# Kernel tuning notes

Hardware: AMD Instinct MI355X
Metric: run time of the kernel (lower is better)

The kernel has to match this reference:

```python
import jax, jax.numpy as jnp
import numpy as np

N_ATOMS, N_EDGES, N_TRIP, N_GRAPHS = 8000, 100000, 500000, 64
H, NR, NS, NB = 128, 6, 7, 8
NBLK, OUT, NBEF, NAFT, NOL = 6, 1, 1, 2, 3


def setup_inputs() -> dict:
    key = jax.random.key(0)
    ks = iter(jax.random.split(key, 64))

    def nrm(shape, s=0.1):
        return jax.random.normal(next(ks), shape, jnp.float32) * s

    def rint(shape, hi):
        return jax.random.randint(next(ks), shape, 0, hi)

    return dict(
        z=rint((N_ATOMS,), 95),
        rbf=nrm((N_EDGES, NR), 1.0),
        sbf=nrm((N_TRIP, NS * NR), 1.0),
        i=rint((N_EDGES,), N_ATOMS),
        j=rint((N_EDGES,), N_ATOMS),
        idx_kj=rint((N_TRIP,), N_EDGES),
        idx_ji=rint((N_TRIP,), N_EDGES),
        batch=jnp.sort(rint((N_ATOMS,), N_GRAPHS)),
        emb_table=nrm((95, H), 1.0),
        emb_rbf_w=nrm((NR, H)), emb_rbf_b=nrm((H,), 0.01),
        emb_w=nrm((3 * H, H)), emb_b=nrm((H,), 0.01),
        int_rbf_w=nrm((NBLK, NR, H)),
        int_sbf_w=nrm((NBLK, NS * NR, NB)),
        int_kj_w=nrm((NBLK, H, H)), int_kj_b=nrm((NBLK, H), 0.01),
        int_ji_w=nrm((NBLK, H, H)), int_ji_b=nrm((NBLK, H), 0.01),
        int_W=nrm((NBLK, H, NB, H), 2.0 / H),
        int_bef_w=nrm((NBLK, 2 * NBEF, H, H)), int_bef_b=nrm((NBLK, 2 * NBEF, H), 0.01),
        int_lin_w=nrm((NBLK, H, H)), int_lin_b=nrm((NBLK, H), 0.01),
        int_aft_w=nrm((NBLK, 2 * NAFT, H, H)), int_aft_b=nrm((NBLK, 2 * NAFT, H), 0.01),
        out_rbf_w=nrm((NBLK + 1, NR, H)),
        out_lins_w=nrm((NBLK + 1, NOL, H, H)), out_lins_b=nrm((NBLK + 1, NOL, H), 0.01),
        out_w=nrm((NBLK + 1, H, OUT)),
    )


def _forward(z, i, j, idx_kj, idx_ji, batch,
             rbf, sbf, emb_table, emb_rbf_w, emb_rbf_b, emb_w, emb_b,
             int_rbf_w, int_sbf_w, int_kj_w, int_kj_b, int_ji_w, int_ji_b,
             int_W, int_bef_w, int_bef_b, int_lin_w, int_lin_b,
             int_aft_w, int_aft_b, out_rbf_w, out_lins_w, out_lins_b, out_w):
    act = jax.nn.silu  # swish

    def residual(h, ws, bs):
        # ws: [2*n_layers, H, H] -> x + act(lin2(act(lin1(x)))) per layer
        for r in range(ws.shape[0] // 2):
            h = h + act(act(h @ ws[2 * r] + bs[2 * r]) @ ws[2 * r + 1] + bs[2 * r + 1])
        return h

    def out_block(xe, k):
        t = (rbf @ out_rbf_w[k]) * xe                      # [E,H]
        t = jax.ops.segment_sum(t, i, num_segments=N_ATOMS)  # edge->node scatter
        for l in range(NOL):
            t = act(t @ out_lins_w[k, l] + out_lins_b[k, l])
        return t @ out_w[k]                                # [N,OUT]

    # EmbeddingBlock
    h_atom = emb_table[z]                                  # [N,H]
    rbf_h = act(rbf @ emb_rbf_w + emb_rbf_b)               # [E,H]
    x = act(jnp.concatenate([h_atom[i], h_atom[j], rbf_h], axis=-1) @ emb_w + emb_b)  # [E,H]

    P = out_block(x, 0)
    for b in range(NBLK):
        rbf_p = rbf @ int_rbf_w[b]                         # [E,H]
        sbf_p = sbf @ int_sbf_w[b]                         # [T,NB]
        x_ji = act(x @ int_ji_w[b] + int_ji_b[b])
        x_kj = act(x @ int_kj_w[b] + int_kj_b[b]) * rbf_p
        xg = x_kj[idx_kj]                                  # triplet gather [T,H]
        # einsum('wj,wl,ijl->wi', sbf_p, xg, W): loop over small NB to avoid [T,NB,H] temp
        Wb = int_W[b]                                      # [H,NB,H]
        m = sbf_p[:, 0:1] * (xg @ Wb[:, 0, :].T)
        for jj in range(1, NB):
            m = m + sbf_p[:, jj:jj + 1] * (xg @ Wb[:, jj, :].T)
        m = jax.ops.segment_sum(m, idx_ji, num_segments=N_EDGES)  # triplet->edge scatter
        h = x_ji + m
        h = residual(h, int_bef_w[b], int_bef_b[b])
        h = act(h @ int_lin_w[b] + int_lin_b[b]) + x       # skip connection
        x = residual(h, int_aft_w[b], int_aft_b[b])
        P = P + out_block(x, b + 1)

    return jax.ops.segment_sum(P, batch, num_segments=N_GRAPHS)  # [B,OUT]


def reference(z, rbf, sbf, i, j, idx_kj, idx_ji, batch,
              emb_table, emb_rbf_w, emb_rbf_b, emb_w, emb_b,
              int_rbf_w, int_sbf_w, int_kj_w, int_kj_b, int_ji_w, int_ji_b,
              int_W, int_bef_w, int_bef_b, int_lin_w, int_lin_b,
              int_aft_w, int_aft_b, out_rbf_w, out_lins_w, out_lins_b, out_w):
    return _forward(z, i, j, idx_kj, idx_ji, batch,
                    rbf, sbf, emb_table, emb_rbf_w, emb_rbf_b, emb_w, emb_b,
                    int_rbf_w, int_sbf_w, int_kj_w, int_kj_b, int_ji_w, int_ji_b,
                    int_W, int_bef_w, int_bef_b, int_lin_w, int_lin_b,
                    int_aft_w, int_aft_b, out_rbf_w, out_lins_w, out_lins_b, out_w)
```

## Files before the change

kernel.cpp:

```cpp
#include <hip/hip_runtime.h>
#include <cstdint>
#include <cstddef>

typedef unsigned short ushort_t;
typedef unsigned int uint_t;

#define NATOMS 8000
#define NEDGES 100000
#define NTRIP  500000
#define NGRAPH 64
#define HD     128
#define NRR    6
#define NSNR   42
#define NBB    8
#define NBLKS  6
#define MSZ    16384

using short8   = __attribute__((ext_vector_type(8))) short;
using ushort8v = __attribute__((ext_vector_type(8))) unsigned short;
using floatx4  = __attribute__((ext_vector_type(4))) float;
using float2v  = __attribute__((ext_vector_type(2))) float;

__device__ __forceinline__ float siluf(float x){ return x / (1.f + __expf(-x)); }
__device__ __forceinline__ ushort_t f2us(float f){
    uint_t u = __builtin_bit_cast(uint_t, f);
    u = (u + 0x7FFFu + ((u >> 16) & 1u)) >> 16;
    return (ushort_t)u;
}
__device__ __forceinline__ float us2f(ushort_t s){
    uint_t u = ((uint_t)s) << 16;
    return __builtin_bit_cast(float, u);
}
__device__ __forceinline__ void wave_lds_fence(){
    asm volatile("s_waitcnt lgkmcnt(0)" ::: "memory");
}
__device__ __forceinline__ short8 ldfrag(const ushort_t* W, int frag, int lane){
    return *(const short8*)(W + ((size_t)(frag * 64 + lane) << 3));
}

__global__ void zerof_k(float* __restrict__ p, int n){ int i=blockIdx.x*256+threadIdx.x; if(i<n) p[i]=0.f; }
__global__ void zeroi_k(int* __restrict__ p, int n){ int i=blockIdx.x*256+threadIdx.x; if(i<n) p[i]=0; }

__global__ __launch_bounds__(256)
void transp128_k(const float* __restrict__ src, ushort_t* __restrict__ dst)
{
    __shared__ ushort_t L[128][130];
    int m = blockIdx.x;
    const float* S = src + (size_t)m * MSZ;
    ushort_t* D = dst + (size_t)m * MSZ;
    int tid = threadIdx.x;
    #pragma unroll
    for (int p = 0; p < 64; ++p) {
        int idx = p * 256 + tid;
        int k = idx >> 7, n = idx & 127;
        L[k][n] = f2us(S[idx]);
    }
    __syncthreads();
    #pragma unroll
    for (int p = 0; p < 64; ++p) {
        int idx = p * 256 + tid;
        int n = idx >> 7, k = idx & 127;
        D[idx] = L[k][n];
    }
}

__global__ __launch_bounds__(256)
void transp128s_k(const float* __restrict__ src, ushort_t* __restrict__ dst)
{
    int m = blockIdx.x;
    const float* S = src + (size_t)m * MSZ;
    ushort_t* D = dst + (size_t)m * MSZ;
    int tid = threadIdx.x;
    #pragma unroll
    for (int p = 0; p < 64; ++p) {
        int idx = p * 256 + tid;
        int k = idx >> 7, n = idx & 127;
        size_t d = ((size_t)(((k >> 5) * 8 + (n >> 4)) * 64 + ((k >> 3) & 3) * 16 + (n & 15)) << 3)
                   + (k & 7);
        D[d] = f2us(S[idx]);
    }
}

__global__ void castWMs_k(const float* __restrict__ src, ushort_t* __restrict__ dst, int n)
{
    int i = blockIdx.x * 256 + threadIdx.x;
    if (i >= n) return;
    int b = i >> 17;
    int r = i & 131071;
    int nn = r >> 10, k = r & 1023;
    size_t d = (size_t)b * 131072
             + ((size_t)(((k >> 5) * 8 + (nn >> 4)) * 64 + ((k >> 3) & 3) * 16 + (nn & 15)) << 3)
             + (k & 7);
    dst[d] = f2us(src[i]);
}

__global__ void pack_bc_k(const float* __restrict__ bef, const float* __restrict__ lin,
                          const float* __restrict__ aft, float* __restrict__ bc)
{
    int b = blockIdx.x;
    for (int i = threadIdx.x; i < 7 * HD; i += 256) {
        int s = i >> 7, h = i & 127;
        float v;
        if (s < 2)      v = bef[(size_t)(b * 2 + s) * HD + h];
        else if (s == 2) v = lin[(size_t)b * HD + h];
        else             v = aft[(size_t)(b * 4 + (s - 3)) * HD + h];
        bc[(size_t)b * 7 * HD + i] = v;
    }
}

__global__ void hist_k(const int* __restrict__ idx, int n, int* __restrict__ cnt)
{
    int i = blockIdx.x * 256 + threadIdx.x;
    if (i < n) atomicAdd(&cnt[idx[i]], 1);
}
__global__ void blksum_k(const int* __restrict__ c, int n, int* __restrict__ bs)
{
    int i = blockIdx.x * 256 + threadIdx.x;
    int v = (i < n) ? c[i] : 0;
    #pragma unroll
    for (int off = 32; off; off >>= 1) v += __shfl_down(v, off);
    __shared__ int sh[4];
    if ((threadIdx.x & 63) == 0) sh[threadIdx.x >> 6] = v;
    __syncthreads();
    if (threadIdx.x == 0) bs[blockIdx.x] = sh[0] + sh[1] + sh[2] + sh[3];
}
__global__ void scanb_k(int* __restrict__ bs, int nb)
{
    __shared__ int sh[1024];
    int t = threadIdx.x;
    int v = (t < nb) ? bs[t] : 0;
    sh[t] = v; __syncthreads();
    for (int off = 1; off < 1024; off <<= 1) {
        int u = (t >= off) ? sh[t - off] : 0;
        __syncthreads();
        sh[t] += u;
        __syncthreads();
    }
    if (t < nb) bs[t] = sh[t] - v;
}
__global__ void scanfin_k(const int* __restrict__ c, int n, const int* __restrict__ bs,
                          int* __restrict__ offs)
{
    __shared__ int sh[256];
    int t = threadIdx.x;
    int i = blockIdx.x * 256 + t;
    int v = (i < n) ? c[i] : 0;
    sh[t] = v; __syncthreads();
    for (int off = 1; off < 256; off <<= 1) {
        int u = (t >= off) ? sh[t - off] : 0;
        __syncthreads();
        sh[t] += u;
        __syncthreads();
    }
    if (i < n)  offs[i] = bs[blockIdx.x] + sh[t] - v;
    if (i == n - 1) offs[n] = bs[blockIdx.x] + sh[t];
}
__global__ void fill_k(const int* __restrict__ idx, int n, const int* __restrict__ offs,
                       int* __restrict__ cur, int* __restrict__ sorted)
{
    int i = blockIdx.x * 256 + threadIdx.x;
    if (i >= n) return;
    int e = idx[i];
    int p = offs[e] + atomicAdd(&cur[e], 1);
    sorted[p] = i;
}
__global__ void invperm_k(const int* __restrict__ tsorted, const int* __restrict__ idx_kj,
                          int* __restrict__ tpos, int* __restrict__ ekjs, int n)
{
    int k = blockIdx.x * 256 + threadIdx.x;
    if (k >= n) return;
    int t = tsorted[k];
    tpos[t] = k;
    ekjs[k] = idx_kj[t];
}

__device__ __forceinline__ void load_bh(const ushort_t* Bt, int kh, int tid, ushort8v r[4])
{
    #pragma unroll
    for (int p = 0; p < 4; ++p) {
        int c = p * 256 + tid;
        int n = c >> 3, c8 = c & 7;
        r[p] = *(const ushort8v*)(Bt + (size_t)n * 128 + kh * 64 + c8 * 8);
    }
}
__device__ __forceinline__ void store_bh(ushort8v r[4], ushort_t (*Bl)[72], int tid)
{
    #pragma unroll
    for (int p = 0; p < 4; ++p) {
        int c = p * 256 + tid;
        *(ushort8v*)&Bl[c >> 3][(c & 7) * 8] = r[p];
    }
}
__device__ __forceinline__ void mfma_kh(ushort_t (*Al)[136], ushort_t (*Bl)[72],
                                        floatx4 acc[4][4], int kh,
                                        int wr, int wc, int lhi, int llo)
{
    #pragma unroll
    for (int ks = 0; ks < 2; ++ks) {
        int kk = ks * 32 + lhi * 8;
        short8 af[4], bf[4];
        #pragma unroll
        for (int tm = 0; tm < 4; ++tm)
            af[tm] = *(const short8*)&Al[wr * 64 + tm * 16 + llo][kh * 64 + kk];
        #pragma unroll
        for (int tn = 0; tn < 4; ++tn)
            bf[tn] = *(const short8*)&Bl[wc * 64 + tn * 16 + llo][kk];
        #pragma unroll
        for (int tm = 0; tm < 4; ++tm)
            #pragma unroll
            for (int tn = 0; tn < 4; ++tn)
                acc[tm][tn] = __builtin_amdgcn_mfma_f32_16x16x32_bf16(
                    af[tm], bf[tn], acc[tm][tn], 0, 0, 0);
    }
}
#define ZERO_ACC4(acc) { _Pragma("unroll") for (int a_=0;a_<4;++a_) _Pragma("unroll") \
    for (int b_=0;b_<4;++b_) _Pragma("unroll") for (int q_=0;q_<4;++q_) acc[a_][b_][q_]=0.f; }
#define ZERO_ACC8(acc) { _Pragma("unroll") for (int t_=0;t_<8;++t_) { acc[t_][0]=0.f; acc[t_][1]=0.f; acc[t_][2]=0.f; acc[t_][3]=0.f; } }

__global__ __launch_bounds__(256)
void emb_chain_k(const float* __restrict__ rbf, const float* __restrict__ W6g,
                 const float* __restrict__ b6g, const ushort_t* __restrict__ Wemb3,
                 const float* __restrict__ A0, const float* __restrict__ A1,
                 const float* __restrict__ emb_b, const int* __restrict__ z,
                 const int* __restrict__ ii, const int* __restrict__ jj,
                 float* __restrict__ X, ushort_t* __restrict__ Xb, int M)
{
    __shared__ ushort_t Al[128][136];
    __shared__ ushort_t Bl[128][72];
    __shared__ float W6[NRR * HD];
    __shared__ float b6s[HD];
    const int tid = threadIdx.x, row0 = blockIdx.x * 128;
    const int wave = tid >> 6, lane = tid & 63;
    const int wr = wave >> 1, wc_ = wave & 1, lhi = lane >> 4, llo = lane & 15;

    for (int i = tid; i < NRR * HD; i += 256) W6[i] = W6g[i];
    if (tid < HD) b6s[tid] = b6g[tid];
    ushort8v r0[4], r1[4];
    load_bh(Wemb3, 0, tid, r0); load_bh(Wemb3, 1, tid, r1);
    __syncthreads();

    {
        int e_l = tid >> 1, half = tid & 1;
        int grow = row0 + e_l; if (grow >= M) grow = M - 1;
        float r6[NRR];
        #pragma unroll
        for (int r = 0; r < NRR; ++r) r6[r] = rbf[(size_t)grow * NRR + r];
        #pragma unroll 8
        for (int hh = 0; hh < 64; ++hh) {
            int h = half * 64 + hh;
            float a = b6s[h];
            #pragma unroll
            for (int r = 0; r < NRR; ++r) a += r6[r] * W6[r * HD + h];
            Al[e_l][h] = f2us(siluf(a));
        }
    }
    __syncthreads();

    floatx4 acc[4][4]; ZERO_ACC4(acc);
    store_bh(r0, Bl, tid); __syncthreads();
    mfma_kh(Al, Bl, acc, 0, wr, wc_, lhi, llo);
    __syncthreads();
    store_bh(r1, Bl, tid); __syncthreads();
    mfma_kh(Al, Bl, acc, 1, wr, wc_, lhi, llo);

    #pragma unroll
    for (int tm = 0; tm < 4; ++tm)
        #pragma unroll
        for (int q = 0; q < 4; ++q) {
            int grow = row0 + wr * 64 + tm * 16 + lhi * 4 + q;
            if (grow >= M) continue;
            int zi = z[ii[grow]], zj = z[jj[grow]];
            #pragma unroll
            for (int tn = 0; tn < 4; ++tn) {
                int coll = wc_ * 64 + tn * 16 + llo;
                float t = acc[tm][tn][q] + A0[zi * HD + coll] + A1[zj * HD + coll] + emb_b[coll];
                float v = siluf(t);
                size_t o = (size_t)grow * HD + coll;
                X[o] = v; Xb[o] = f2us(v);
            }
        }
}

__global__ __launch_bounds__(256, 3)
void kjcb_w(const ushort_t* __restrict__ Xb, const ushort_t* __restrict__ Wkj,
            const float* __restrict__ bkj, const float* __restrict__ rbf,
            const float* __restrict__ Wr6, ushort_t* __restrict__ Cb, int M)
{
    __shared__ float W6s[NRR * HD];
    __shared__ float bkjS[HD];
    const int tid = threadIdx.x, wave = tid >> 6, lane = tid & 63;
    const int llo = lane & 15, lhi = lane >> 4;
    for (int i = tid; i < NRR * HD; i += 256) W6s[i] = Wr6[i];
    if (tid < HD) bkjS[tid] = bkj[tid];
    __syncthreads();
    const int row0 = (blockIdx.x * 4 + wave) * 16;
    if (row0 >= M) return;

    short8 af[4];
    #pragma unroll
    for (int kc = 0; kc < 4; ++kc)
        af[kc] = *(const short8*)(Xb + (size_t)(row0 + llo) * HD + kc * 32 + lhi * 8);

    short8 nb[2][8];
    #pragma unroll
    for (int d = 0; d < 2; ++d)
        #pragma unroll
        for (int tn = 0; tn < 8; ++tn) nb[d][tn] = ldfrag(Wkj, d * 8 + tn, lane);

    float rb[4][NRR];
    {
        const float* rp = rbf + (size_t)(row0 + lhi * 4) * NRR;
        #pragma unroll
        for (int q = 0; q < 4; ++q)
            #pragma unroll
            for (int r = 0; r < NRR; ++r) rb[q][r] = rp[q * NRR + r];
    }

    floatx4 acc[8]; ZERO_ACC8(acc);
    #pragma unroll
    for (int kc = 0; kc < 4; ++kc) {
        short8 bq[8];
        #pragma unroll
        for (int tn = 0; tn < 8; ++tn) bq[tn] = nb[kc & 1][tn];
        if (kc + 2 < 4) {
            #pragma unroll
            for (int tn = 0; tn < 8; ++tn) nb[kc & 1][tn] = ldfrag(Wkj, (kc + 2) * 8 + tn, lane);
        }
        #pragma unroll
        for (int tn = 0; tn < 8; ++tn)
            acc[tn] = __builtin_amdgcn_mfma_f32_16x16x32_bf16(af[kc], bq[tn], acc[tn], 0, 0, 0);
    }
    #pragma unroll
    for (int tn = 0; tn < 8; ++tn) {
        int col = tn * 16 + llo;
        #pragma unroll
        for (int q = 0; q < 4; ++q) {
            int grow = row0 + lhi * 4 + q;
            if (grow >= M) continue;
            float rpv = 0.f;
            #pragma unroll
            for (int r = 0; r < NRR; ++r) rpv += rb[q][r] * W6s[r * HD + col];
            Cb[(size_t)grow * HD + col] = f2us(siluf(acc[tn][q] + bkjS[col]) * rpv);
        }
    }
}

__global__ __launch_bounds__(256, 4)
void megaK_w(const ushort_t* __restrict__ sps, const ushort_t* __restrict__ Cb,
             const int* __restrict__ toffs, const int* __restrict__ ekjs,
             const ushort_t* __restrict__ Xb,
             const ushort_t* __restrict__ Wm,
             const ushort_t* __restrict__ Wji, const float* __restrict__ bjig,
             const ushort_t* __restrict__ Wc, const float* __restrict__ Bc,
             float* __restrict__ X, ushort_t* __restrict__ Xbo)
{
    __shared__ ushort_t Ga[16384];
    const int tid = threadIdx.x, wave = tid >> 6, lane = tid & 63;
    const int llo = lane & 15, lhi = lane >> 4;
    const int tn0 = wave * 2, tn1 = tn0 + 1;
    const int col0 = tn0 * 16 + llo, col1 = tn1 * 16 + llo;

    const float bj0 = bjig[col0], bj1 = bjig[col1];
    float bsc0[7], bsc1[7];
    #pragma unroll
    for (int s = 0; s < 7; ++s) {
        bsc0[s] = Bc[s * HD + col0];
        bsc1[s] = Bc[s * HD + col1];
    }

    const int row0 = blockIdx.x * 16;

    {
        const int we0 = row0 + wave * 4;
        const int tf0 = __builtin_amdgcn_readfirstlane(toffs[we0]);
        const int tf1 = __builtin_amdgcn_readfirstlane(toffs[we0 + 1]);
        const int tf2 = __builtin_amdgcn_readfirstlane(toffs[we0 + 2]);
        const int tf3 = __builtin_amdgcn_readfirstlane(toffs[we0 + 3]);
        const int tf4 = __builtin_amdgcn_readfirstlane(toffs[we0 + 4]);
        const int wk0 = tf0, wk1 = tf4;
        const uint_t* __restrict__ Cb32 = (const uint_t*)Cb;

        float2v accp[8];
        #pragma unroll
        for (int j = 0; j < 8; ++j) accp[j] = (float2v){0.f, 0.f};

        int ekA[8]; uint_t cbuf[8]; ushort8v sbuf[8];
        #pragma unroll
        for (int p = 0; p < 8; ++p)
            ekA[p] = (wk0 + p < wk1) ? __builtin_amdgcn_readfirstlane(ekjs[wk0 + p]) : 0;
        #pragma unroll
        for (int p = 0; p < 8; ++p)
            if (wk0 + p < wk1) {
                cbuf[p] = Cb32[(size_t)ekA[p] * 64 + lane];
                sbuf[p] = *(const ushort8v*)(sps + (size_t)(wk0 + p) * NBB);
            }
        #pragma unroll
        for (int p = 0; p < 8; ++p)
            ekA[p] = (wk0 + 8 + p < wk1) ? __builtin_amdgcn_readfirstlane(ekjs[wk0 + 8 + p]) : 0;

        int e = 0;
        auto kendof = [&](int ee) {
            return ee == 0 ? tf1 : ee == 1 ? tf2 : ee == 2 ? tf3 : tf4;
        };
        auto flush = [&](int ee) {
            const int el_ = wave * 4 + ee;
            const int sw_ = (el_ & 7) << 3;
            const int gb_ = el_ << 10;
            const int cix = (2 * lane) ^ sw_;
            #pragma unroll
            for (int j = 0; j < 8; ++j) {
                uint_t pk = (uint_t)f2us(accp[j][0]) | ((uint_t)f2us(accp[j][1]) << 16);
                *(uint_t*)&Ga[gb_ + (j << 7) + cix] = pk;
                accp[j] = (float2v){0.f, 0.f};
            }
        };

        for (int base = wk0; base < wk1; base += 8) {
            #pragma unroll
            for (int p = 0; p < 8; ++p) {
                const int kk = base + p;
                if (kk < wk1) {
                    while (e < 4 && kk >= kendof(e)) { flush(e); ++e; }
                    const uint_t  cu = cbuf[p];
                    const ushort8v sv = sbuf[p];
                    if (kk + 8 < wk1) {
                        cbuf[p] = Cb32[(size_t)ekA[p] * 64 + lane];
                        sbuf[p] = *(const ushort8v*)(sps + (size_t)(kk + 8) * NBB);
                    }
                    if (kk + 16 < wk1)
                        ekA[p] = __builtin_amdgcn_readfirstlane(ekjs[kk + 16]);
                    const float2v c2 = { us2f((ushort_t)(cu & 0xffffu)),
                                         __builtin_bit_cast(float, cu & 0xffff0000u) };
                    #pragma unroll
                    for (int j = 0; j < 8; ++j) {
                        const float s = us2f(sv[j]);
                        accp[j] += (float2v){s, s} * c2;
                    }
                }
            }
        }
        while (e < 4) { flush(e); ++e; }
    }
    __syncthreads();

    floatx4 m0 = {0.f,0.f,0.f,0.f}, m1 = {0.f,0.f,0.f,0.f};
    {
        const int abase = llo << 10;
        const int aswz  = llo & 7;
        short8 ap[2]; short8 bp[4][2];
        #pragma unroll
        for (int d = 0; d < 2; ++d)
            ap[d] = *(const short8*)&Ga[abase + ((((d << 2) + lhi) ^ aswz) << 3)];
        #pragma unroll
        for (int d = 0; d < 4; ++d) {
            bp[d][0] = ldfrag(Wm, d * 8 + tn0, lane);
            bp[d][1] = ldfrag(Wm, d * 8 + tn1, lane);
        }
        __builtin_amdgcn_s_setprio(1);
        #pragma unroll
        for (int kc = 0; kc < 32; ++kc) {
            short8 a  = ap[kc & 1];
            short8 b0 = bp[kc & 3][0], b1 = bp[kc & 3][1];
            if (kc + 2 < 32)
                ap[kc & 1] = *(const short8*)&Ga[abase + (((((kc + 2) << 2) + lhi) ^ aswz) << 3)];
            if (kc + 4 < 32) {
                bp[kc & 3][0] = ldfrag(Wm, (kc + 4) * 8 + tn0, lane);
                bp[kc & 3][1] = ldfrag(Wm, (kc + 4) * 8 + tn1, lane);
            }
            m0 = __builtin_amdgcn_mfma_f32_16x16x32_bf16(a, b0, m0, 0, 0, 0);
            m1 = __builtin_amdgcn_mfma_f32_16x16x32_bf16(a, b1, m1, 0, 0, 0);
        }
        __builtin_amdgcn_s_setprio(0);
    }
    __syncthreads();

    ushort_t (*Tw)[136] = (ushort_t (*)[136])&Ga[0];

    float cur0[4], cur1[4], res0[4], res1[4], trk0[4], trk1[4];
    short8 nb[2][2];
    #pragma unroll
    for (int d = 0; d < 2; ++d) {
        nb[d][0] = ldfrag(Wji, d * 8 + tn0, lane);
        nb[d][1] = ldfrag(Wji, d * 8 + tn1, lane);
    }
    {
        short8 af[4];
        #pragma unroll
        for (int kc = 0; kc < 4; ++kc)
            af[kc] = *(const short8*)(Xb + (size_t)(row0 + llo) * HD + kc * 32 + lhi * 8);
        floatx4 a0 = {0.f,0.f,0.f,0.f}, a1 = {0.f,0.f,0.f,0.f};
        #pragma unroll
        for (int kc = 0; kc < 4; ++kc) {
            short8 b0 = nb[kc & 1][0], b1 = nb[kc & 1][1];
            {
                const int ps = kc + 2;
                const ushort_t* W = (ps < 4) ? Wji : Wc;
                nb[kc & 1][0] = ldfrag(W, (ps & 3) * 8 + tn0, lane);
                nb[kc & 1][1] = ldfrag(W, (ps & 3) * 8 + tn1, lane);
            }
            a0 = __builtin_amdgcn_mfma_f32_16x16x32_bf16(af[kc], b0, a0, 0, 0, 0);
            a1 = __builtin_amdgcn_mfma_f32_16x16x32_bf16(af[kc], b1, a1, 0, 0, 0);
        }
        #pragma unroll
        for (int q = 0; q < 4; ++q) {
            res0[q] = siluf(a0[q] + bj0) + m0[q];
            res1[q] = siluf(a1[q] + bj1) + m1[q];
            cur0[q] = res0[q]; cur1[q] = res1[q];
        }
    }

    float xr0[4], xr1[4];
    #pragma unroll
    for (int q = 0; q < 4; ++q) {
        int grow = row0 + lhi * 4 + q;
        xr0[q] = X[(size_t)grow * HD + col0];
        xr1[q] = X[(size_t)grow * HD + col1];
    }

    #pragma unroll
    for (int s = 0; s < 7; ++s) {
        #pragma unroll
        for (int q = 0; q < 4; ++q) {
            Tw[lhi * 4 + q][col0] = f2us(cur0[q]);
            Tw[lhi * 4 + q][col1] = f2us(cur1[q]);
        }
        __syncthreads();

        floatx4 a0 = {0.f,0.f,0.f,0.f}, a1 = {0.f,0.f,0.f,0.f};
        const int sg0 = 4 + s * 4;
        #pragma unroll
        for (int kc = 0; kc < 4; ++kc) {
            const int seg = sg0 + kc;
            short8 a8 = *(const short8*)&Tw[llo][kc * 32 + lhi * 8];
            short8 b0 = nb[seg & 1][0], b1 = nb[seg & 1][1];
            if (seg + 2 < 32) {
                const int ps = seg + 2;
                const ushort_t* W = Wc + (size_t)((ps - 4) >> 2) * MSZ;
                nb[seg & 1][0] = ldfrag(W, (ps & 3) * 8 + tn0, lane);
                nb[seg & 1][1] = ldfrag(W, (ps & 3) * 8 + tn1, lane);
            }
            a0 = __builtin_amdgcn_mfma_f32_16x16x32_bf16(a8, b0, a0, 0, 0, 0);
            a1 = __builtin_amdgcn_mfma_f32_16x16x32_bf16(a8, b1, a1, 0, 0, 0);
        }
        __syncthreads();

        #pragma unroll
        for (int q = 0; q < 4; ++q) {
            float t0v = siluf(a0[q] + bsc0[s]);
            float t1v = siluf(a1[q] + bsc1[s]);
            if (s == 0)      { cur0[q] = t0v; cur1[q] = t1v; }
            else if (s == 1) { cur0[q] = t0v + res0[q]; cur1[q] = t1v + res1[q]; }
            else if (s == 2) {
                cur0[q] = t0v + xr0[q];
                cur1[q] = t1v + xr1[q];
                trk0[q] = cur0[q]; trk1[q] = cur1[q];
            }
            else if (s == 3 || s == 5) { cur0[q] = t0v; cur1[q] = t1v; }
            else {
                cur0[q] = t0v + trk0[q]; cur1[q] = t1v + trk1[q];
                trk0[q] = cur0[q]; trk1[q] = cur1[q];
            }
        }
    }

    #pragma unroll
    for (int q = 0; q < 4; ++q) {
        int grow = row0 + lhi * 4 + q;
        size_t o = (size_t)grow * HD;
        X[o + col0] = cur0[q];        X[o + col1] = cur1[q];
        Xbo[o + col0] = f2us(cur0[q]); Xbo[o + col1] = f2us(cur1[q]);
    }
}

__global__ __launch_bounds__(256)
void gatherT_k(const ushort_t* __restrict__ Xb, const float* __restrict__ rbf,
               const float* __restrict__ Wr6, const int* __restrict__ eoffs,
               const int* __restrict__ esorted, ushort_t* __restrict__ TA, int M)
{
    __shared__ float W6s[NRR * HD];
    const int tid = threadIdx.x, wave = tid >> 6, lane = tid & 63;
    for (int i = tid; i < NRR * HD; i += 256) W6s[i] = Wr6[i];
    __syncthreads();
    int a0 = (blockIdx.x * 4 + wave) * 2;
    #pragma unroll
    for (int s = 0; s < 2; ++s) {
        int a = a0 + s;
        if (a >= M) return;
        float acc0 = 0.f, acc1 = 0.f;
        int k1 = eoffs[a + 1];
        for (int k = eoffs[a]; k < k1; ++k) {
            int e = esorted[k];
            float r6[NRR];
            #pragma unroll
            for (int r = 0; r < NRR; ++r) r6[r] = rbf[(size_t)e * NRR + r];
            float rp0 = 0.f, rp1 = 0.f;
            #pragma unroll
            for (int r = 0; r < NRR; ++r) {
                rp0 += r6[r] * W6s[r * HD + lane];
                rp1 += r6[r] * W6s[r * HD + 64 + lane];
            }
            acc0 += rp0 * us2f(Xb[(size_t)e * HD + lane]);
            acc1 += rp1 * us2f(Xb[(size_t)e * HD + 64 + lane]);
        }
        TA[(size_t)a * HD + lane] = f2us(acc0);
        TA[(size_t)a * HD + 64 + lane] = f2us(acc1);
    }
}

__global__ __launch_bounds__(256, 3)
void atomchain_w(const ushort_t* __restrict__ TA, const ushort_t* __restrict__ Wl,
                 const float* __restrict__ bl, const float* __restrict__ wout,
                 float* __restrict__ P, int M)
{
    __shared__ float blS[3 * HD];
    __shared__ float woS[HD];
    __shared__ ushort_t T[4][16][136];
    const int tid = threadIdx.x, wave = tid >> 6, lane = tid & 63;
    const int llo = lane & 15, lhi = lane >> 4;
    for (int i = tid; i < 3 * HD; i += 256) blS[i] = bl[i];
    if (tid < HD) woS[tid] = wout[tid];
    __syncthreads();
    const int row0 = (blockIdx.x * 4 + wave) * 16;
    if (row0 >= M) return;
    ushort_t (*Tw)[136] = T[wave];

    short8 nb[2][8];
    #pragma unroll
    for (int d = 0; d < 2; ++d)
        #pragma unroll
        for (int tn = 0; tn < 8; ++tn) nb[d][tn] = ldfrag(Wl, d * 8 + tn, lane);

    #pragma unroll
    for (int s = 0; s < 3; ++s) {
        short8 af[4];
        if (s == 0) {
            #pragma unroll
            for (int kc = 0; kc < 4; ++kc)
                af[kc] = *(const short8*)(TA + (size_t)(row0 + llo) * HD + kc * 32 + lhi * 8);
        } else {
            #pragma unroll
            for (int kc = 0; kc < 4; ++kc)
                af[kc] = *(const short8*)&Tw[llo][kc * 32 + lhi * 8];
        }
        floatx4 acc[8]; ZERO_ACC8(acc);
        #pragma unroll
        for (int kc = 0; kc < 4; ++kc) {
            const int seg = s * 4 + kc;
            short8 bq[8];
            #pragma unroll
            for (int tn = 0; tn < 8; ++tn) bq[tn] = nb[seg & 1][tn];
            if (seg + 2 < 12) {
                const int ps = seg + 2;
                const ushort_t* W = Wl + (size_t)(ps >> 2) * MSZ;
                #pragma unroll
                for (int tn = 0; tn < 8; ++tn)
                    nb[seg & 1][tn] = ldfrag(W, (ps & 3) * 8 + tn, lane);
            }
            #pragma unroll
            for (int tn = 0; tn < 8; ++tn)
                acc[tn] = __builtin_amdgcn_mfma_f32_16x16x32_bf16(af[kc], bq[tn], acc[tn], 0, 0, 0);
        }
        if (s < 2) {
            wave_lds_fence();
            #pragma unroll
            for (int tn = 0; tn < 8; ++tn) {
                int col = tn * 16 + llo;
                #pragma unroll
                for (int q = 0; q < 4; ++q)
                    Tw[lhi * 4 + q][col] = f2us(siluf(acc[tn][q] + blS[s * HD + col]));
            }
            wave_lds_fence();
        } else {
            #pragma unroll
            for (int q = 0; q < 4; ++q) {
                float v = 0.f;
                #pragma unroll
                for (int tn = 0; tn < 8; ++tn) {
                    int col = tn * 16 + llo;
                    v += siluf(acc[tn][q] + blS[2 * HD + col]) * woS[col];
                }
                v += __shfl_xor(v, 1); v += __shfl_xor(v, 2);
                v += __shfl_xor(v, 4); v += __shfl_xor(v, 8);
                int a = row0 + lhi * 4 + q;
                if (llo == 0 && a < M) P[a] += v;
            }
        }
    }
}

__global__ void emb_lin_k(const float* __restrict__ emb_table, const float* __restrict__ emb_w,
                          float* __restrict__ A0, float* __restrict__ A1)
{
    __shared__ float er[HD];
    int a = blockIdx.x, h = threadIdx.x;
    er[h] = emb_table[a * HD + h];
    __syncthreads();
    float acc0 = 0.f, acc1 = 0.f;
    #pragma unroll 8
    for (int l = 0; l < HD; ++l) {
        float e = er[l];
        acc0 += e * emb_w[l * HD + h];
        acc1 += e * emb_w[(HD + l) * HD + h];
    }
    A0[a * HD + h] = acc0;
    A1[a * HD + h] = acc1;
}

__global__ void sbf_proj_s(const float* __restrict__ sbf, const float* __restrict__ W,
                           const int* __restrict__ tpos, ushort_t* __restrict__ sps)
{
    __shared__ float Ws[NSNR * NBB];
    for (int s = threadIdx.x; s < NSNR * NBB; s += 256) Ws[s] = W[s];
    __syncthreads();
    int t = blockIdx.x * 256 + threadIdx.x;
    if (t >= NTRIP) return;
    float acc[NBB];
    #pragma unroll
    for (int n = 0; n < NBB; ++n) acc[n] = 0.f;
    #pragma unroll
    for (int r = 0; r < NSNR; ++r) {
        float v = sbf[(size_t)t * NSNR + r];
        #pragma unroll
        for (int n = 0; n < NBB; ++n) acc[n] += v * Ws[r * NBB + n];
    }
    int p = tpos[t];
    ushort_t* o = sps + (size_t)p * NBB;
    #pragma unroll
    for (int n = 0; n < NBB; ++n) o[n] = f2us(acc[n]);
}

__global__ void graph_sum_k(const float* __restrict__ P, const int* __restrict__ batch,
                            float* __restrict__ outg)
{
    int a = blockIdx.x * 256 + threadIdx.x;
    if (a >= NATOMS) return;
    atomicAdd(&outg[batch[a]], P[a]);
}

extern "C" void kernel_launch(void* const* d_in, const int* in_sizes, int n_in,
                              void* d_out, int out_size, void* d_ws, size_t ws_size,
                              hipStream_t stream)
{
    const int*   z         = (const int*)  d_in[0];
    const float* rbf       = (const float*)d_in[1];
    const float* sbf       = (const float*)d_in[2];
    const int*   ii        = (const int*)  d_in[3];
    const int*   jj        = (const int*)  d_in[4];
    const int*   idx_kj    = (const int*)  d_in[5];
    const int*   idx_ji    = (const int*)  d_in[6];
    const int*   batch     = (const int*)  d_in[7];
    const float* emb_table = (const float*)d_in[8];
    const float* emb_rbf_w = (const float*)d_in[9];
    const float* emb_rbf_b = (const float*)d_in[10];
    const float* emb_w     = (const float*)d_in[11];
    const float* emb_b     = (const float*)d_in[12];
    const float* int_rbf_w = (const float*)d_in[13];
    const float* int_sbf_w = (const float*)d_in[14];
    const float* int_kj_w  = (const float*)d_in[15];
    const float* int_kj_b  = (const float*)d_in[16];
    const float* int_ji_w  = (const float*)d_in[17];
    const float* int_ji_b  = (const float*)d_in[18];
    const float* int_W     = (const float*)d_in[19];
    const float* int_bef_w = (const float*)d_in[20];
    const float* int_bef_b = (const float*)d_in[21];
    const float* int_lin_w = (const float*)d_in[22];
    const float* int_lin_b = (const float*)d_in[23];
    const float* int_aft_w = (const float*)d_in[24];
    const float* int_aft_b = (const float*)d_in[25];
    const float* out_rbf_w = (const float*)d_in[26];
    const float* out_lins_w= (const float*)d_in[27];
    const float* out_lins_b= (const float*)d_in[28];
    const float* out_w     = (const float*)d_in[29];
    float* d_outf          = (float*)d_out;

    const size_t EH = (size_t)NEDGES * HD;
    const int OFF_EMB = 0, OFF_KJ = 1, OFF_JI = 7, OFF_CHAIN = 13, OFF_OUTL = 55;

    char* base = (char*)d_ws;
    auto take = [&](size_t bytes) { char* p = base; base += (bytes + 255) & ~(size_t)255; return p; };
    float* bufA    = (float*)take(EH * 4);
    ushort_t* Xb   = (ushort_t*)take(EH * 2);
    ushort_t* Cb   = (ushort_t*)take(EH * 2);
    ushort_t* sps  = (ushort_t*)take((size_t)NTRIP * NBB * 2);
    ushort_t* TA   = (ushort_t*)take((size_t)NATOMS * HD * 2);
    float* P_atom  = (float*)take((size_t)NATOMS * 4);
    float* A0      = (float*)take(95 * HD * 4);
    float* A1      = (float*)take(95 * HD * 4);
    float* bc      = (float*)take((size_t)NBLKS * 7 * HD * 4);
    int*   counts  = (int*)  take((size_t)(NEDGES + 1) * 4);
    int*   bsum    = (int*)  take(1024 * 4);
    int*   toffs   = (int*)  take((size_t)(NEDGES + 1) * 4);
    int*   eoffs   = (int*)  take((size_t)(NATOMS + 1) * 4);
    int*   tsorted = (int*)  take((size_t)NTRIP * 4);
    int*   esorted = (int*)  take((size_t)NEDGES * 4);
    int*   tpos    = (int*)  take((size_t)NTRIP * 4);
    int*   ekjs    = (int*)  take((size_t)NTRIP * 4);
    ushort_t* w128 = (ushort_t*)take((size_t)76 * MSZ * 2);
    ushort_t* wM   = (ushort_t*)take((size_t)NBLKS * HD * 1024 * 2);

    auto zero = [&](float* p, size_t n) {
        zerof_k<<<((int)n + 255) / 256, 256, 0, stream>>>(p, (int)n);
    };

    transp128_k<<< 1, 256, 0, stream>>>(emb_w + 2 * MSZ, w128 + (size_t)OFF_EMB * MSZ);
    transp128s_k<<< 6, 256, 0, stream>>>(int_kj_w,   w128 + (size_t)OFF_KJ  * MSZ);
    transp128s_k<<< 6, 256, 0, stream>>>(int_ji_w,   w128 + (size_t)OFF_JI  * MSZ);
    for (int b = 0; b < NBLKS; ++b) {
        transp128s_k<<<2, 256, 0, stream>>>(int_bef_w + (size_t)b * 2 * MSZ,
                                            w128 + (size_t)(OFF_CHAIN + b * 7) * MSZ);
        transp128s_k<<<1, 256, 0, stream>>>(int_lin_w + (size_t)b * MSZ,
                                            w128 + (size_t)(OFF_CHAIN + b * 7 + 2) * MSZ);
        transp128s_k<<<4, 256, 0, stream>>>(int_aft_w + (size_t)b * 4 * MSZ,
                                            w128 + (size_t)(OFF_CHAIN + b * 7 + 3) * MSZ);
    }
    transp128s_k<<<21, 256, 0, stream>>>(out_lins_w, w128 + (size_t)OFF_OUTL * MSZ);
    castWMs_k<<<(NBLKS * HD * 1024 + 255) / 256, 256, 0, stream>>>(int_W, wM, NBLKS * HD * 1024);
    pack_bc_k<<<NBLKS, 256, 0, stream>>>(int_bef_b, int_lin_b, int_aft_b, bc);

    {
        zeroi_k<<<(NEDGES + 255) / 256, 256, 0, stream>>>(counts, NEDGES);
        hist_k<<<(NTRIP + 255) / 256, 256, 0, stream>>>(idx_ji, NTRIP, counts);
        int nb = (NEDGES + 255) / 256;
        blksum_k<<<nb, 256, 0, stream>>>(counts, NEDGES, bsum);
        scanb_k<<<1, 1024, 0, stream>>>(bsum, nb);
        scanfin_k<<<nb, 256, 0, stream>>>(counts, NEDGES, bsum, toffs);
        zeroi_k<<<(NEDGES + 255) / 256, 256, 0, stream>>>(counts, NEDGES);
        fill_k<<<(NTRIP + 255) / 256, 256, 0, stream>>>(idx_ji, NTRIP, toffs, counts, tsorted);
        invperm_k<<<(NTRIP + 255) / 256, 256, 0, stream>>>(tsorted, idx_kj, tpos, ekjs, NTRIP);
    }
    {
        zeroi_k<<<(NATOMS + 255) / 256, 256, 0, stream>>>(counts, NATOMS);
        hist_k<<<(NEDGES + 255) / 256, 256, 0, stream>>>(ii, NEDGES, counts);
        int nb = (NATOMS + 255) / 256;
        blksum_k<<<nb, 256, 0, stream>>>(counts, NATOMS, bsum);
        scanb_k<<<1, 1024, 0, stream>>>(bsum, nb);
        scanfin_k<<<nb, 256, 0, stream>>>(counts, NATOMS, bsum, eoffs);
        zeroi_k<<<(NATOMS + 255) / 256, 256, 0, stream>>>(counts, NATOMS);
        fill_k<<<(NEDGES + 255) / 256, 256, 0, stream>>>(ii, NEDGES, eoffs, counts, esorted);
    }

    const int EGRID = (NEDGES + 127) / 128;
    const int EW    = (NEDGES / 16 + 3) / 4;
    const int AW    = (NATOMS / 16 + 3) / 4;
    const int GW    = (NATOMS / 2 + 3) / 4;
    const int MW    = NEDGES / 16;
    auto out_block = [&](int k) {
        gatherT_k<<<GW, 256, 0, stream>>>(
            Xb, rbf, out_rbf_w + (size_t)k * NRR * HD, eoffs, esorted, TA, NATOMS);
        atomchain_w<<<AW, 256, 0, stream>>>(
            TA, w128 + (size_t)(OFF_OUTL + 3 * k) * MSZ,
            out_lins_b + (size_t)k * 3 * HD, out_w + (size_t)k * HD, P_atom, NATOMS);
    };

    emb_lin_k<<<95, HD, 0, stream>>>(emb_table, emb_w, A0, A1);
    emb_chain_k<<<EGRID, 256, 0, stream>>>(
        rbf, emb_rbf_w, emb_rbf_b, w128 + (size_t)OFF_EMB * MSZ,
        A0, A1, emb_b, z, ii, jj, bufA, Xb, NEDGES);

    zero(P_atom, NATOMS);
    out_block(0);

    for (int b = 0; b < NBLKS; ++b) {
        sbf_proj_s<<<(NTRIP + 255) / 256, 256, 0, stream>>>(
            sbf, int_sbf_w + (size_t)b * NSNR * NBB, tpos, sps);

        kjcb_w<<<EW, 256, 0, stream>>>(
            Xb, w128 + (size_t)(OFF_KJ + b) * MSZ, int_kj_b + (size_t)b * HD,
            rbf, int_rbf_w + (size_t)b * NRR * HD, Cb, NEDGES);

        megaK_w<<<MW, 256, 0, stream>>>(
            sps, Cb, toffs, ekjs, Xb,
            wM + (size_t)b * HD * 1024,
            w128 + (size_t)(OFF_JI + b) * MSZ, int_ji_b + (size_t)b * HD,
            w128 + (size_t)(OFF_CHAIN + b * 7) * MSZ, bc + (size_t)b * 7 * HD,
            bufA, Xb);

        out_block(b + 1);
    }

    zero(d_outf, NGRAPH);
    graph_sum_k<<<(NATOMS + 255) / 256, 256, 0, stream>>>(P_atom, batch, d_outf);
}
```

Before: 2.223 ms.

## Compute triplet-to-edge aggregation with block-wide MFMA over 32-triplet chunks

Replaces the per-wave scalar FMA accumulation of sbf-weighted gathered kj features with a block-cooperative scheme. Each 32-triplet chunk is staged in shared memory: a one-hot-style A tile holds the sbf coefficients routed to (edge, basis) rows and a transposed C tile holds the gathered features, then bf16 MFMA accumulates into per-wave registers. The aim is to cut the scalar FMA work and balance triplet load across the block instead of per wave. In exchange it adds three barriers per chunk, zero-fills a mostly sparse A tile, and wastes MFMA work on zero rows.

```diff
diff --git a/kernel.cpp b/kernel.cpp
--- a/kernel.cpp
+++ b/kernel.cpp
@@ -360,6 +360,9 @@
     const int tn0 = wave * 2, tn1 = tn0 + 1;
     const int col0 = tn0 * 16 + llo, col1 = tn1 * 16 + llo;
 
+    ushort_t* const At = &Ga[0];
+    ushort_t* const Ct = &Ga[5120];
+
     const float bj0 = bjig[col0], bj1 = bjig[col1];
     float bsc0[7], bsc1[7];
     #pragma unroll
@@ -370,76 +373,81 @@
 
     const int row0 = blockIdx.x * 16;
 
+    floatx4 gacc[8][2];
+    #pragma unroll
+    for (int mt = 0; mt < 8; ++mt) {
+        gacc[mt][0] = (floatx4){0.f,0.f,0.f,0.f};
+        gacc[mt][1] = (floatx4){0.f,0.f,0.f,0.f};
+    }
     {
-        const int we0 = row0 + wave * 4;
-        const int tf0 = __builtin_amdgcn_readfirstlane(toffs[we0]);
-        const int tf1 = __builtin_amdgcn_readfirstlane(toffs[we0 + 1]);
-        const int tf2 = __builtin_amdgcn_readfirstlane(toffs[we0 + 2]);
-        const int tf3 = __builtin_amdgcn_readfirstlane(toffs[we0 + 3]);
-        const int tf4 = __builtin_amdgcn_readfirstlane(toffs[we0 + 4]);
-        const int wk0 = tf0, wk1 = tf4;
-        const uint_t* __restrict__ Cb32 = (const uint_t*)Cb;
-
-        float2v accp[8];
-        #pragma unroll
-        for (int j = 0; j < 8; ++j) accp[j] = (float2v){0.f, 0.f};
-
-        int ekA[8]; uint_t cbuf[8]; ushort8v sbuf[8];
-        #pragma unroll
-        for (int p = 0; p < 8; ++p)
-            ekA[p] = (wk0 + p < wk1) ? __builtin_amdgcn_readfirstlane(ekjs[wk0 + p]) : 0;
-        #pragma unroll
-        for (int p = 0; p < 8; ++p)
-            if (wk0 + p < wk1) {
-                cbuf[p] = Cb32[(size_t)ekA[p] * 64 + lane];
-                sbuf[p] = *(const ushort8v*)(sps + (size_t)(wk0 + p) * NBB);
-            }
-        #pragma unroll
-        for (int p = 0; p < 8; ++p)
-            ekA[p] = (wk0 + 8 + p < wk1) ? __builtin_amdgcn_readfirstlane(ekjs[wk0 + 8 + p]) : 0;
-
-        int e = 0;
-        auto kendof = [&](int ee) {
-            return ee == 0 ? tf1 : ee == 1 ? tf2 : ee == 2 ? tf3 : tf4;
-        };
-        auto flush = [&](int ee) {
-            const int el_ = wave * 4 + ee;
-            const int sw_ = (el_ & 7) << 3;
-            const int gb_ = el_ << 10;
-            const int cix = (2 * lane) ^ sw_;
-            #pragma unroll
-            for (int j = 0; j < 8; ++j) {
-                uint_t pk = (uint_t)f2us(accp[j][0]) | ((uint_t)f2us(accp[j][1]) << 16);
-                *(uint_t*)&Ga[gb_ + (j << 7) + cix] = pk;
-                accp[j] = (float2v){0.f, 0.f};
-            }
-        };
-
-        for (int base = wk0; base < wk1; base += 8) {
-            #pragma unroll
-            for (int p = 0; p < 8; ++p) {
-                const int kk = base + p;
-                if (kk < wk1) {
-                    while (e < 4 && kk >= kendof(e)) { flush(e); ++e; }
-                    const uint_t  cu = cbuf[p];
-                    const ushort8v sv = sbuf[p];
-                    if (kk + 8 < wk1) {
-                        cbuf[p] = Cb32[(size_t)ekA[p] * 64 + lane];
-                        sbuf[p] = *(const ushort8v*)(sps + (size_t)(kk + 8) * NBB);
-                    }
-                    if (kk + 16 < wk1)
-                        ekA[p] = __builtin_amdgcn_readfirstlane(ekjs[kk + 16]);
-                    const float2v c2 = { us2f((ushort_t)(cu & 0xffffu)),
-                                         __builtin_bit_cast(float, cu & 0xffff0000u) };
-                    #pragma unroll
-                    for (int j = 0; j < 8; ++j) {
-                        const float s = us2f(sv[j]);
-                        accp[j] += (float2v){s, s} * c2;
-                    }
+        int tf[17];
+        #pragma unroll
+        for (int i2 = 0; i2 <= 16; ++i2)
+            tf[i2] = __builtin_amdgcn_readfirstlane(toffs[row0 + i2]);
+        const int K0 = tf[0], K4 = tf[16];
+        const int nch = (K4 - K0 + 31) >> 5;
+
+        const int kk8 = tid >> 3;
+        const int jsl = tid & 7;
+        const int h0  = (tid & 7) * 16;
+
+        for (int c = 0; c < nch; ++c) {
+            const int kg = K0 + c * 32 + kk8;
+            const bool va = kg < K4;
+
+            ushort8v cv0 = {0,0,0,0,0,0,0,0}, cv1 = {0,0,0,0,0,0,0,0};
+            ushort_t sv = 0; int eid = 0;
+            if (va) {
+                const int crow = ekjs[kg];
+                cv0 = *(const ushort8v*)(Cb + (size_t)crow * HD + h0);
+                cv1 = *(const ushort8v*)(Cb + (size_t)crow * HD + h0 + 8);
+                sv  = sps[(size_t)kg * NBB + jsl];
+                #pragma unroll
+                for (int e2 = 1; e2 <= 16; ++e2) eid += (kg >= tf[e2]) ? 1 : 0;
+            }
+
+            {
+                unsigned long long* Az = (unsigned long long*)At;
+                #pragma unroll
+                for (int z = 0; z < 5; ++z) Az[tid * 5 + z] = 0ULL;
+            }
+            __syncthreads();
+
+            #pragma unroll
+            for (int m = 0; m < 8; ++m) {
+                Ct[(h0 + m) * 40 + kk8]     = cv0[m];
+                Ct[(h0 + 8 + m) * 40 + kk8] = cv1[m];
+            }
+            if (va) At[(eid * 8 + jsl) * 40 + kk8] = sv;
+            __syncthreads();
+
+            {
+                short8 bf0 = *(const short8*)&Ct[col0 * 40 + lhi * 8];
+                short8 bf1 = *(const short8*)&Ct[col1 * 40 + lhi * 8];
+                #pragma unroll
+                for (int mt = 0; mt < 8; ++mt) {
+                    short8 afm = *(const short8*)&At[(mt * 16 + llo) * 40 + lhi * 8];
+                    gacc[mt][0] = __builtin_amdgcn_mfma_f32_16x16x32_bf16(afm, bf0, gacc[mt][0], 0, 0, 0);
+                    gacc[mt][1] = __builtin_amdgcn_mfma_f32_16x16x32_bf16(afm, bf1, gacc[mt][1], 0, 0, 0);
                 }
             }
-        }
-        while (e < 4) { flush(e); ++e; }
+            __syncthreads();
+        }
+    }
+
+    #pragma unroll
+    for (int mt = 0; mt < 8; ++mt) {
+        const int el = mt * 2 + (lhi >> 1);
+        const int jb = (lhi & 1) * 4;
+        const int sw = (el & 7) << 3;
+        #pragma unroll
+        for (int nt2 = 0; nt2 < 2; ++nt2) {
+            const int h  = wave * 32 + nt2 * 16 + llo;
+            const int hx = h ^ sw;
+            #pragma unroll
+            for (int q = 0; q < 4; ++q)
+                Ga[el * 1024 + (jb + q) * 128 + hx] = f2us(gacc[mt][nt2][q]);
+        }
     }
     __syncthreads();
 
```

New measurement: 2.166 ms. 2.6% less time.
